# Kernel optimization log

Measured on AMD Instinct MI355X. Metric: run time of the kernel, lower is better.

## Reference

```python
import jax, jax.numpy as jnp
import numpy as np

N = 100000      # nodes
E = 1600000     # edges (avg degree 16)
IN, HID, OUT = 64, 64, 32
R = 8           # relations


def setup_inputs() -> dict:
    key = jax.random.key(0)
    ks = jax.random.split(key, 8)
    s = jnp.float32(0.05)  # weight init scale
    return {
        "feat": jax.random.normal(ks[0], (N, IN), dtype=jnp.float32),
        "src": jax.random.randint(ks[1], (E,), 0, N),
        "dst": jax.random.randint(ks[2], (E,), 0, N),
        "etypes": jax.random.randint(ks[3], (E,), 0, R),
        "W1": jax.random.normal(ks[4], (R, IN, HID), dtype=jnp.float32) * s,
        "Wself1": jax.random.normal(ks[5], (IN, HID), dtype=jnp.float32) * s,
        "b1": jnp.zeros((HID,), jnp.float32),
        "W2": jax.random.normal(ks[6], (R, HID, OUT), dtype=jnp.float32) * s,
        "Wself2": jax.random.normal(ks[7], (HID, OUT), dtype=jnp.float32) * s,
        "b2": jnp.zeros((OUT,), jnp.float32),
    }


def _rel_graph_conv(h, src, dst, etypes, W, Wself, b):
    """RelGraphConv with sum aggregation, self-loop and bias.

    h: [N, din], W: [R, din, dout], Wself: [din, dout], b: [dout].
    """
    n = h.shape[0]
    # Transform all nodes by all relation weights once: [R, N, dout].
    hW = jnp.einsum('nd,rdo->rno', h, W)
    # Per-edge message: relation-specific transform of the source node.
    msg = hW[etypes, src]                                    # [E, dout]
    # Scatter-add messages to destination nodes.
    agg = jax.ops.segment_sum(msg, dst, num_segments=n)      # [N, dout]
    return agg + h @ Wself + b


def reference(feat, src, dst, etypes, W1, Wself1, b1, W2, Wself2, b2):
    x = jax.nn.relu(_rel_graph_conv(feat, src, dst, etypes, W1, Wself1, b1))
    return _rel_graph_conv(x, src, dst, etypes, W2, Wself2, b2)
```

## Files before the change

kernel.cpp:

```cpp
#include <hip/hip_runtime.h>
#include <hip/hip_bf16.h>

typedef __attribute__((ext_vector_type(8))) short short8;
typedef __attribute__((ext_vector_type(4))) float f32x4;

__device__ __forceinline__ unsigned short f2bf(float v) {
    __hip_bfloat16 h = __float2bfloat16(v);
    return *reinterpret_cast<unsigned short*>(&h);
}
__device__ __forceinline__ float bf2f(unsigned short u) {
    union { unsigned int i; float f; } x;
    x.i = (unsigned int)u << 16;
    return x.f;
}

constexpr int MAXB = 2048;

template<int H>
__global__ __launch_bounds__(256) void transpose_w(
    const float* __restrict__ W, const float* __restrict__ Wself,
    unsigned short* __restrict__ Wt, int R)
{
    int i = blockIdx.x * 256 + threadIdx.x;
    int total = (R + 1) * H * 64;
    if (i >= total) return;
    int d = i & 63;
    int hh = i >> 6;
    int r = hh / H, h = hh % H;
    float v = (r < R) ? W[((size_t)r * 64 + d) * H + h]
                      : Wself[(size_t)d * H + h];
    Wt[i] = f2bf(v);
}

template<int H, int RT, bool ABF, bool SBF>
__global__ __launch_bounds__(512) void gemm_rel_mfma(
    const void* __restrict__ Av, const unsigned short* __restrict__ Wt,
    const float* __restrict__ bias,
    unsigned short* __restrict__ C, void* __restrict__ Cselfv,
    int N, int Rrt, int relu)
{
    constexpr int AS = 72;
    __shared__ unsigned short As[64 * AS];
    const int R = RT ? RT : Rrt;
    const int tid = threadIdx.x;
    const int n0 = blockIdx.x * 64;

    if constexpr (ABF) {
        const unsigned short* A = (const unsigned short*)Av;
        int n = tid >> 3, d8 = (tid & 7) * 8;
        int gn = n0 + n;
        short8 u = {};
        if (gn < N) u = *(const short8*)&A[(size_t)gn * 64 + d8];
        if (relu) {
            #pragma unroll
            for (int j = 0; j < 8; ++j) {
                unsigned short x = (unsigned short)u[j];
                u[j] = (short)((x & 0x8000) ? 0 : x);
            }
        }
        *(short8*)&As[n * AS + d8] = u;
    } else {
        const float* A = (const float*)Av;
        #pragma unroll
        for (int i = 0; i < 2; ++i) {
            int lin = tid + i * 512;
            int n = lin >> 4;
            int d4 = (lin & 15) * 4;
            int gn = n0 + n;
            float4 v = make_float4(0.f, 0.f, 0.f, 0.f);
            if (gn < N) v = *(const float4*)&A[(size_t)gn * 64 + d4];
            if (relu) {
                v.x = fmaxf(v.x, 0.f); v.y = fmaxf(v.y, 0.f);
                v.z = fmaxf(v.z, 0.f); v.w = fmaxf(v.w, 0.f);
            }
            ushort4 u;
            u.x = f2bf(v.x); u.y = f2bf(v.y); u.z = f2bf(v.z); u.w = f2bf(v.w);
            *(ushort4*)&As[n * AS + d4] = u;
        }
    }

    const int w = tid >> 6, lane = tid & 63;
    const int m = lane & 15, quad = lane >> 4;
    const int wt = w & 3;
    const int half = w >> 2;
    const int node = n0 + wt * 16 + m;

    __syncthreads();

    short8 afrag[2];
    afrag[0] = *(const short8*)&As[(wt * 16 + m) * AS + 0 * 32 + quad * 8];
    afrag[1] = *(const short8*)&As[(wt * 16 + m) * AS + 1 * 32 + quad * 8];

    constexpr int NT = H / 32;

    auto wptr = [&](int r, int nt, int kc) {
        int colbase = half * (H / 2) + nt * 16;
        return (const short8*)&Wt[((size_t)(r * H + colbase + m)) * 64 + kc * 32 + quad * 8];
    };

    short8 wf0[NT][2], wf1[NT][2];
    #pragma unroll
    for (int nt = 0; nt < NT; ++nt) { wf0[nt][0] = *wptr(0, nt, 0); wf0[nt][1] = *wptr(0, nt, 1); }
    #pragma unroll
    for (int nt = 0; nt < NT; ++nt) { wf1[nt][0] = *wptr(1, nt, 0); wf1[nt][1] = *wptr(1, nt, 1); }

    #pragma unroll
    for (int r = 0; r <= R; ++r) {
        short8 wn[NT][2];
        if (r + 2 <= R) {
            #pragma unroll
            for (int nt = 0; nt < NT; ++nt) {
                wn[nt][0] = *wptr(r + 2, nt, 0);
                wn[nt][1] = *wptr(r + 2, nt, 1);
            }
        }

        f32x4 acc[NT];
        #pragma unroll
        for (int nt = 0; nt < NT; ++nt) {
            acc[nt] = (f32x4){0.f, 0.f, 0.f, 0.f};
            acc[nt] = __builtin_amdgcn_mfma_f32_16x16x32_bf16(wf0[nt][0], afrag[0], acc[nt], 0, 0, 0);
            acc[nt] = __builtin_amdgcn_mfma_f32_16x16x32_bf16(wf0[nt][1], afrag[1], acc[nt], 0, 0, 0);
        }

        if (r < R) {
            #pragma unroll
            for (int nt = 0; nt < NT; ++nt) {
                int colbase = half * (H / 2) + nt * 16;
                if (node < N) {
                    ushort4 u;
                    u.x = f2bf(acc[nt][0]); u.y = f2bf(acc[nt][1]);
                    u.z = f2bf(acc[nt][2]); u.w = f2bf(acc[nt][3]);
                    *(ushort4*)&C[((size_t)r * N + node) * H + colbase + quad * 4] = u;
                }
            }
        } else {
            #pragma unroll
            for (int nt = 0; nt < NT; ++nt) {
                int colbase = half * (H / 2) + nt * 16;
                if (node < N) {
                    float4 bv = *(const float4*)&bias[colbase + quad * 4];
                    if constexpr (SBF) {
                        unsigned short* Cs = (unsigned short*)Cselfv;
                        ushort4 u;
                        u.x = f2bf(acc[nt][0] + bv.x); u.y = f2bf(acc[nt][1] + bv.y);
                        u.z = f2bf(acc[nt][2] + bv.z); u.w = f2bf(acc[nt][3] + bv.w);
                        *(ushort4*)&Cs[(size_t)node * H + colbase + quad * 4] = u;
                    } else {
                        float* Cs = (float*)Cselfv;
                        float4 o = make_float4(acc[nt][0] + bv.x, acc[nt][1] + bv.y,
                                               acc[nt][2] + bv.z, acc[nt][3] + bv.w);
                        *(float4*)&Cs[(size_t)node * H + colbase + quad * 4] = o;
                    }
                }
            }
        }

        #pragma unroll
        for (int nt = 0; nt < NT; ++nt) {
            wf0[nt][0] = wf1[nt][0]; wf0[nt][1] = wf1[nt][1];
            wf1[nt][0] = wn[nt][0];  wf1[nt][1] = wn[nt][1];
        }
    }
}

__global__ __launch_bounds__(256) void zero_int(int* __restrict__ p, int n) {
    int i = blockIdx.x * 256 + threadIdx.x;
    if (i < n) p[i] = 0;
}

__global__ __launch_bounds__(256) void fine_hist(
    const int* __restrict__ dst, int* __restrict__ ghist, int E, int B, int CH)
{
    __shared__ int hist[MAXB];
    const int t = threadIdx.x;
    const int e0 = blockIdx.x * CH, e1 = min(E, e0 + CH);
    for (int i = t; i < B; i += 256) hist[i] = 0;
    __syncthreads();
    for (int e = e0 + t; e < e1; e += 256) atomicAdd(&hist[dst[e] >> 6], 1);
    __syncthreads();
    for (int i = t; i < B; i += 256) {
        int h = hist[i];
        if (h) atomicAdd(&ghist[i], h);
    }
}

__global__ __launch_bounds__(256) void fine_scan(
    const int* __restrict__ ghist, int* __restrict__ bstart,
    int* __restrict__ cursor, int B, int E)
{
    __shared__ int ts[256];
    const int t = threadIdx.x;
    const int PER = (B + 255) / 256;
    int loc[8];
    int s = 0;
    for (int j = 0; j < PER; ++j) {
        int i = t * PER + j;
        loc[j] = (i < B) ? ghist[i] : 0;
        s += loc[j];
    }
    ts[t] = s;
    __syncthreads();
    for (int off = 1; off < 256; off <<= 1) {
        int x = (t >= off) ? ts[t - off] : 0;
        __syncthreads();
        ts[t] += x;
        __syncthreads();
    }
    int run = ts[t] - s;
    for (int j = 0; j < PER; ++j) {
        int i = t * PER + j;
        if (i < B) { bstart[i] = run; cursor[i] = run; }
        run += loc[j];
    }
    if (t == 255) bstart[B] = E;
}

__global__ __launch_bounds__(256) void partition_fine(
    const int* __restrict__ src, const int* __restrict__ dst,
    const int* __restrict__ et, int* __restrict__ cursor,
    int* __restrict__ rec, int E, int N, int B, int CH)
{
    __shared__ int hist[MAXB];
    __shared__ int base[MAXB];
    __shared__ int cnt[MAXB];
    const int t = threadIdx.x;
    const int e0 = blockIdx.x * CH, e1 = min(E, e0 + CH);

    for (int i = t; i < B; i += 256) hist[i] = 0;
    __syncthreads();
    for (int e = e0 + t; e < e1; e += 256) atomicAdd(&hist[dst[e] >> 6], 1);
    __syncthreads();
    for (int i = t; i < B; i += 256) {
        int h = hist[i];
        base[i] = h ? atomicAdd(&cursor[i], h) : 0;
        cnt[i] = 0;
    }
    __syncthreads();
    for (int e = e0 + t; e < e1; e += 256) {
        int d = dst[e];
        int b = d >> 6;
        int pos = base[b] + atomicAdd(&cnt[b], 1);
        rec[pos] = ((et[e] * N + src[e]) << 6) | (d & 63);
    }
}

__global__ __launch_bounds__(256) void bucket_sort(
    const int* __restrict__ bstart, const int* __restrict__ rec,
    int* __restrict__ eidx, int* __restrict__ row_ptr, int N, int E)
{
    __shared__ int hist[64];
    __shared__ int excl[64];
    __shared__ int cur[64];
    const int b = blockIdx.x;
    const int tid = threadIdx.x;
    const int p0 = bstart[b], p1 = bstart[b + 1];

    if (tid < 64) hist[tid] = 0;
    __syncthreads();
    for (int p = p0 + tid; p < p1; p += 256)
        atomicAdd(&hist[rec[p] & 63], 1);
    __syncthreads();
    if (tid == 0) {
        int run = 0;
        #pragma unroll
        for (int i = 0; i < 64; ++i) { excl[i] = run; run += hist[i]; }
    }
    __syncthreads();
    if (tid < 64) {
        cur[tid] = excl[tid];
        int n = b * 64 + tid;
        if (n < N) row_ptr[n] = p0 + excl[tid];
    }
    if (b == 0 && tid == 0) row_ptr[N] = E;
    __syncthreads();
    for (int p = p0 + tid; p < p1; p += 256) {
        int rv = rec[p];
        int pos = p0 + atomicAdd(&cur[rv & 63], 1);
        eidx[pos] = rv >> 6;
    }
}

__global__ __launch_bounds__(256) void agg_csr64(
    const unsigned int* __restrict__ hw32, const int* __restrict__ row_ptr,
    const int* __restrict__ eidx, unsigned int* __restrict__ out32, int N)
{
    const int d = blockIdx.x * 4 + (threadIdx.x >> 6);
    const int lane = threadIdx.x & 63;
    if (d >= N) return;
    const int he = lane >> 5;
    const int c = lane & 31;
    const int p0 = row_ptr[d], p1 = row_ptr[d + 1];
    float s0 = 0.f, s1 = 0.f, t0 = 0.f, t1 = 0.f;
    int p = p0 + he;
    for (; p + 6 < p1; p += 8) {
        unsigned int v0 = hw32[(size_t)eidx[p]     * 32 + c];
        unsigned int v1 = hw32[(size_t)eidx[p + 2] * 32 + c];
        unsigned int v2 = hw32[(size_t)eidx[p + 4] * 32 + c];
        unsigned int v3 = hw32[(size_t)eidx[p + 6] * 32 + c];
        s0 += bf2f((unsigned short)(v0 & 0xffff)); s1 += bf2f((unsigned short)(v0 >> 16));
        t0 += bf2f((unsigned short)(v1 & 0xffff)); t1 += bf2f((unsigned short)(v1 >> 16));
        s0 += bf2f((unsigned short)(v2 & 0xffff)); s1 += bf2f((unsigned short)(v2 >> 16));
        t0 += bf2f((unsigned short)(v3 & 0xffff)); t1 += bf2f((unsigned short)(v3 >> 16));
    }
    for (; p < p1; p += 2) {
        unsigned int v = hw32[(size_t)eidx[p] * 32 + c];
        s0 += bf2f((unsigned short)(v & 0xffff)); s1 += bf2f((unsigned short)(v >> 16));
    }
    s0 += t0; s1 += t1;
    float u0 = __shfl(s0, c + 32, 64);
    float u1 = __shfl(s1, c + 32, 64);
    if (he == 0) {
        unsigned int cur = out32[(size_t)d * 32 + c];
        float o0 = s0 + u0 + bf2f((unsigned short)(cur & 0xffff));
        float o1 = s1 + u1 + bf2f((unsigned short)(cur >> 16));
        out32[(size_t)d * 32 + c] = (unsigned int)f2bf(o0) | ((unsigned int)f2bf(o1) << 16);
    }
}

__global__ __launch_bounds__(256) void agg_csr32(
    const unsigned int* __restrict__ hw32, const int* __restrict__ row_ptr,
    const int* __restrict__ eidx, float* __restrict__ out, int N)
{
    const int d = blockIdx.x * 8 + (threadIdx.x >> 5);
    const int l = threadIdx.x & 31;
    if (d >= N) return;
    const int he = l >> 4;
    const int c = l & 15;
    const int p0 = row_ptr[d], p1 = row_ptr[d + 1];
    float s0 = 0.f, s1 = 0.f, t0 = 0.f, t1 = 0.f;
    int p = p0 + he;
    for (; p + 6 < p1; p += 8) {
        unsigned int v0 = hw32[(size_t)eidx[p]     * 16 + c];
        unsigned int v1 = hw32[(size_t)eidx[p + 2] * 16 + c];
        unsigned int v2 = hw32[(size_t)eidx[p + 4] * 16 + c];
        unsigned int v3 = hw32[(size_t)eidx[p + 6] * 16 + c];
        s0 += bf2f((unsigned short)(v0 & 0xffff)); s1 += bf2f((unsigned short)(v0 >> 16));
        t0 += bf2f((unsigned short)(v1 & 0xffff)); t1 += bf2f((unsigned short)(v1 >> 16));
        s0 += bf2f((unsigned short)(v2 & 0xffff)); s1 += bf2f((unsigned short)(v2 >> 16));
        t0 += bf2f((unsigned short)(v3 & 0xffff)); t1 += bf2f((unsigned short)(v3 >> 16));
    }
    for (; p < p1; p += 2) {
        unsigned int v = hw32[(size_t)eidx[p] * 16 + c];
        s0 += bf2f((unsigned short)(v & 0xffff)); s1 += bf2f((unsigned short)(v >> 16));
    }
    s0 += t0; s1 += t1;
    float u0 = __shfl(s0, (threadIdx.x & 63) ^ 16, 64);
    float u1 = __shfl(s1, (threadIdx.x & 63) ^ 16, 64);
    if (he == 0) {
        float2 cur = *(const float2*)&out[(size_t)d * 32 + c * 2];
        float2 o = make_float2(cur.x + s0 + u0, cur.y + s1 + u1);
        *(float2*)&out[(size_t)d * 32 + c * 2] = o;
    }
}

extern "C" void kernel_launch(void* const* d_in, const int* in_sizes, int n_in,
                              void* d_out, int out_size, void* d_ws, size_t ws_size,
                              hipStream_t stream)
{
    const float* feat = (const float*)d_in[0];
    const int*   src  = (const int*)d_in[1];
    const int*   dst  = (const int*)d_in[2];
    const int*   et   = (const int*)d_in[3];
    const float* W1   = (const float*)d_in[4];
    const float* Ws1  = (const float*)d_in[5];
    const float* b1   = (const float*)d_in[6];
    const float* W2   = (const float*)d_in[7];
    const float* Ws2  = (const float*)d_in[8];
    const float* b2   = (const float*)d_in[9];
    float* out = (float*)d_out;

    const int N = in_sizes[0] / 64;
    const int E = in_sizes[1];
    const int R = in_sizes[4] / (64 * 64);
    const int B = (N + 63) / 64;

    unsigned short* hW  = (unsigned short*)d_ws;
    unsigned short* h1  = hW + (size_t)R * N * 64;
    unsigned short* Wt1 = h1 + (size_t)N * 64;
    unsigned short* Wt2 = Wt1 + (size_t)(R + 1) * 64 * 64;
    int*   ghist   = (int*)(Wt2 + (size_t)(R + 1) * 32 * 64);
    int*   bstart  = ghist + B;
    int*   cursor  = bstart + (B + 1);
    int*   row_ptr = cursor + B;
    int*   rec     = row_ptr + (N + 1);
    int*   eidx    = rec + E;

    const dim3 blk(256);
    const int nblk64 = (N + 63) / 64;
    const int P  = 128;
    const int CH = (E + P - 1) / P;

    transpose_w<64><<<((R + 1) * 64 * 64 + 255) / 256, blk, 0, stream>>>(W1, Ws1, Wt1, R);
    transpose_w<32><<<((R + 1) * 32 * 64 + 255) / 256, blk, 0, stream>>>(W2, Ws2, Wt2, R);

    zero_int<<<(B + 255) / 256, blk, 0, stream>>>(ghist, B);
    fine_hist<<<P, blk, 0, stream>>>(dst, ghist, E, B, CH);
    fine_scan<<<1, blk, 0, stream>>>(ghist, bstart, cursor, B, E);
    partition_fine<<<P, blk, 0, stream>>>(src, dst, et, cursor, rec, E, N, B, CH);
    bucket_sort<<<B, blk, 0, stream>>>(bstart, rec, eidx, row_ptr, N, E);

    if (R == 8)
        gemm_rel_mfma<64, 8, false, true><<<nblk64, 512, 0, stream>>>(feat, Wt1, b1, hW, h1, N, R, 0);
    else
        gemm_rel_mfma<64, 0, false, true><<<nblk64, 512, 0, stream>>>(feat, Wt1, b1, hW, h1, N, R, 0);
    agg_csr64<<<dim3((N + 3) / 4), blk, 0, stream>>>((const unsigned int*)hW, row_ptr, eidx,
                                                     (unsigned int*)h1, N);

    if (R == 8)
        gemm_rel_mfma<32, 8, true, false><<<nblk64, 512, 0, stream>>>(h1, Wt2, b2, hW, out, N, R, 1);
    else
        gemm_rel_mfma<32, 0, true, false><<<nblk64, 512, 0, stream>>>(h1, Wt2, b2, hW, out, N, R, 1);
    agg_csr32<<<dim3((N + 7) / 8), blk, 0, stream>>>((const unsigned int*)hW, row_ptr, eidx, out, N);
}
```

Before: 396.3 us.

## Aggregate source features per relation before transform, fusing gather and GEMM

Reorders the RGCN layer to aggregate raw bf16 source features per (destination tile, relation) into shared memory with LDS atomics, then multiply by each relation weight with MFMA. This drops materialising the R×N×H transformed-feature tensor and its separate gather pass. Edges are bucketed by destination tile and then by relation, and the packed record now stores etype in high bits. The cost is shared-memory atomics, many block syncs per relation, and bf16 rounding of the partial sums before the MFMA.

```diff
diff --git a/kernel.cpp b/kernel.cpp
--- a/kernel.cpp
+++ b/kernel.cpp
@@ -15,6 +15,7 @@
 }
 
 constexpr int MAXB = 2048;
+constexpr int SP   = 66;
 
 template<int H>
 __global__ __launch_bounds__(256) void transpose_w(
@@ -32,136 +33,19 @@
     Wt[i] = f2bf(v);
 }
 
-template<int H, int RT, bool ABF, bool SBF>
-__global__ __launch_bounds__(512) void gemm_rel_mfma(
-    const void* __restrict__ Av, const unsigned short* __restrict__ Wt,
-    const float* __restrict__ bias,
-    unsigned short* __restrict__ C, void* __restrict__ Cselfv,
-    int N, int Rrt, int relu)
-{
-    constexpr int AS = 72;
-    __shared__ unsigned short As[64 * AS];
-    const int R = RT ? RT : Rrt;
-    const int tid = threadIdx.x;
-    const int n0 = blockIdx.x * 64;
-
-    if constexpr (ABF) {
-        const unsigned short* A = (const unsigned short*)Av;
-        int n = tid >> 3, d8 = (tid & 7) * 8;
-        int gn = n0 + n;
-        short8 u = {};
-        if (gn < N) u = *(const short8*)&A[(size_t)gn * 64 + d8];
-        if (relu) {
-            #pragma unroll
-            for (int j = 0; j < 8; ++j) {
-                unsigned short x = (unsigned short)u[j];
-                u[j] = (short)((x & 0x8000) ? 0 : x);
-            }
-        }
-        *(short8*)&As[n * AS + d8] = u;
-    } else {
-        const float* A = (const float*)Av;
-        #pragma unroll
-        for (int i = 0; i < 2; ++i) {
-            int lin = tid + i * 512;
-            int n = lin >> 4;
-            int d4 = (lin & 15) * 4;
-            int gn = n0 + n;
-            float4 v = make_float4(0.f, 0.f, 0.f, 0.f);
-            if (gn < N) v = *(const float4*)&A[(size_t)gn * 64 + d4];
-            if (relu) {
-                v.x = fmaxf(v.x, 0.f); v.y = fmaxf(v.y, 0.f);
-                v.z = fmaxf(v.z, 0.f); v.w = fmaxf(v.w, 0.f);
-            }
-            ushort4 u;
-            u.x = f2bf(v.x); u.y = f2bf(v.y); u.z = f2bf(v.z); u.w = f2bf(v.w);
-            *(ushort4*)&As[n * AS + d4] = u;
-        }
-    }
-
-    const int w = tid >> 6, lane = tid & 63;
-    const int m = lane & 15, quad = lane >> 4;
-    const int wt = w & 3;
-    const int half = w >> 2;
-    const int node = n0 + wt * 16 + m;
-
-    __syncthreads();
-
-    short8 afrag[2];
-    afrag[0] = *(const short8*)&As[(wt * 16 + m) * AS + 0 * 32 + quad * 8];
-    afrag[1] = *(const short8*)&As[(wt * 16 + m) * AS + 1 * 32 + quad * 8];
-
-    constexpr int NT = H / 32;
-
-    auto wptr = [&](int r, int nt, int kc) {
-        int colbase = half * (H / 2) + nt * 16;
-        return (const short8*)&Wt[((size_t)(r * H + colbase + m)) * 64 + kc * 32 + quad * 8];
-    };
-
-    short8 wf0[NT][2], wf1[NT][2];
-    #pragma unroll
-    for (int nt = 0; nt < NT; ++nt) { wf0[nt][0] = *wptr(0, nt, 0); wf0[nt][1] = *wptr(0, nt, 1); }
-    #pragma unroll
-    for (int nt = 0; nt < NT; ++nt) { wf1[nt][0] = *wptr(1, nt, 0); wf1[nt][1] = *wptr(1, nt, 1); }
-
-    #pragma unroll
-    for (int r = 0; r <= R; ++r) {
-        short8 wn[NT][2];
-        if (r + 2 <= R) {
-            #pragma unroll
-            for (int nt = 0; nt < NT; ++nt) {
-                wn[nt][0] = *wptr(r + 2, nt, 0);
-                wn[nt][1] = *wptr(r + 2, nt, 1);
-            }
-        }
-
-        f32x4 acc[NT];
-        #pragma unroll
-        for (int nt = 0; nt < NT; ++nt) {
-            acc[nt] = (f32x4){0.f, 0.f, 0.f, 0.f};
-            acc[nt] = __builtin_amdgcn_mfma_f32_16x16x32_bf16(wf0[nt][0], afrag[0], acc[nt], 0, 0, 0);
-            acc[nt] = __builtin_amdgcn_mfma_f32_16x16x32_bf16(wf0[nt][1], afrag[1], acc[nt], 0, 0, 0);
-        }
-
-        if (r < R) {
-            #pragma unroll
-            for (int nt = 0; nt < NT; ++nt) {
-                int colbase = half * (H / 2) + nt * 16;
-                if (node < N) {
-                    ushort4 u;
-                    u.x = f2bf(acc[nt][0]); u.y = f2bf(acc[nt][1]);
-                    u.z = f2bf(acc[nt][2]); u.w = f2bf(acc[nt][3]);
-                    *(ushort4*)&C[((size_t)r * N + node) * H + colbase + quad * 4] = u;
-                }
-            }
-        } else {
-            #pragma unroll
-            for (int nt = 0; nt < NT; ++nt) {
-                int colbase = half * (H / 2) + nt * 16;
-                if (node < N) {
-                    float4 bv = *(const float4*)&bias[colbase + quad * 4];
-                    if constexpr (SBF) {
-                        unsigned short* Cs = (unsigned short*)Cselfv;
-                        ushort4 u;
-                        u.x = f2bf(acc[nt][0] + bv.x); u.y = f2bf(acc[nt][1] + bv.y);
-                        u.z = f2bf(acc[nt][2] + bv.z); u.w = f2bf(acc[nt][3] + bv.w);
-                        *(ushort4*)&Cs[(size_t)node * H + colbase + quad * 4] = u;
-                    } else {
-                        float* Cs = (float*)Cselfv;
-                        float4 o = make_float4(acc[nt][0] + bv.x, acc[nt][1] + bv.y,
-                                               acc[nt][2] + bv.z, acc[nt][3] + bv.w);
-                        *(float4*)&Cs[(size_t)node * H + colbase + quad * 4] = o;
-                    }
-                }
-            }
-        }
-
-        #pragma unroll
-        for (int nt = 0; nt < NT; ++nt) {
-            wf0[nt][0] = wf1[nt][0]; wf0[nt][1] = wf1[nt][1];
-            wf1[nt][0] = wn[nt][0];  wf1[nt][1] = wn[nt][1];
-        }
-    }
+__global__ __launch_bounds__(256) void cast_bf16x8(
+    const float* __restrict__ in, unsigned short* __restrict__ outp, int n8)
+{
+    int i = blockIdx.x * 256 + threadIdx.x;
+    if (i >= n8) return;
+    const float4 a = ((const float4*)in)[(size_t)i * 2];
+    const float4 b = ((const float4*)in)[(size_t)i * 2 + 1];
+    short8 u;
+    u[0] = (short)f2bf(a.x); u[1] = (short)f2bf(a.y);
+    u[2] = (short)f2bf(a.z); u[3] = (short)f2bf(a.w);
+    u[4] = (short)f2bf(b.x); u[5] = (short)f2bf(b.y);
+    u[6] = (short)f2bf(b.z); u[7] = (short)f2bf(b.w);
+    *(short8*)&outp[(size_t)i * 8] = u;
 }
 
 __global__ __launch_bounds__(256) void zero_int(int* __restrict__ p, int n) {
@@ -241,116 +125,205 @@
         int d = dst[e];
         int b = d >> 6;
         int pos = base[b] + atomicAdd(&cnt[b], 1);
-        rec[pos] = ((et[e] * N + src[e]) << 6) | (d & 63);
-    }
-}
-
-__global__ __launch_bounds__(256) void bucket_sort(
+        rec[pos] = (et[e] << 23) | (src[e] << 6) | (d & 63);
+    }
+}
+
+__global__ __launch_bounds__(256) void bucket_sort_rel(
     const int* __restrict__ bstart, const int* __restrict__ rec,
-    int* __restrict__ eidx, int* __restrict__ row_ptr, int N, int E)
-{
-    __shared__ int hist[64];
-    __shared__ int excl[64];
-    __shared__ int cur[64];
+    int* __restrict__ eidx, int* __restrict__ brp, int R)
+{
+    __shared__ int hist[16];
+    __shared__ int excl[17];
+    __shared__ int cur[16];
     const int b = blockIdx.x;
     const int tid = threadIdx.x;
     const int p0 = bstart[b], p1 = bstart[b + 1];
 
-    if (tid < 64) hist[tid] = 0;
+    if (tid < 16) hist[tid] = 0;
     __syncthreads();
     for (int p = p0 + tid; p < p1; p += 256)
-        atomicAdd(&hist[rec[p] & 63], 1);
+        atomicAdd(&hist[rec[p] >> 23], 1);
     __syncthreads();
     if (tid == 0) {
         int run = 0;
-        #pragma unroll
-        for (int i = 0; i < 64; ++i) { excl[i] = run; run += hist[i]; }
-    }
-    __syncthreads();
-    if (tid < 64) {
-        cur[tid] = excl[tid];
-        int n = b * 64 + tid;
-        if (n < N) row_ptr[n] = p0 + excl[tid];
-    }
-    if (b == 0 && tid == 0) row_ptr[N] = E;
+        for (int i = 0; i < R; ++i) { excl[i] = run; run += hist[i]; }
+        excl[R] = run;
+    }
+    __syncthreads();
+    if (tid <= R) {
+        brp[b * (R + 1) + tid] = p0 + excl[tid];
+        if (tid < R) cur[tid] = excl[tid];
+    }
     __syncthreads();
     for (int p = p0 + tid; p < p1; p += 256) {
         int rv = rec[p];
-        int pos = p0 + atomicAdd(&cur[rv & 63], 1);
-        eidx[pos] = rv >> 6;
-    }
-}
-
-__global__ __launch_bounds__(256) void agg_csr64(
-    const unsigned int* __restrict__ hw32, const int* __restrict__ row_ptr,
-    const int* __restrict__ eidx, unsigned int* __restrict__ out32, int N)
-{
-    const int d = blockIdx.x * 4 + (threadIdx.x >> 6);
-    const int lane = threadIdx.x & 63;
-    if (d >= N) return;
-    const int he = lane >> 5;
-    const int c = lane & 31;
-    const int p0 = row_ptr[d], p1 = row_ptr[d + 1];
-    float s0 = 0.f, s1 = 0.f, t0 = 0.f, t1 = 0.f;
-    int p = p0 + he;
-    for (; p + 6 < p1; p += 8) {
-        unsigned int v0 = hw32[(size_t)eidx[p]     * 32 + c];
-        unsigned int v1 = hw32[(size_t)eidx[p + 2] * 32 + c];
-        unsigned int v2 = hw32[(size_t)eidx[p + 4] * 32 + c];
-        unsigned int v3 = hw32[(size_t)eidx[p + 6] * 32 + c];
-        s0 += bf2f((unsigned short)(v0 & 0xffff)); s1 += bf2f((unsigned short)(v0 >> 16));
-        t0 += bf2f((unsigned short)(v1 & 0xffff)); t1 += bf2f((unsigned short)(v1 >> 16));
-        s0 += bf2f((unsigned short)(v2 & 0xffff)); s1 += bf2f((unsigned short)(v2 >> 16));
-        t0 += bf2f((unsigned short)(v3 & 0xffff)); t1 += bf2f((unsigned short)(v3 >> 16));
-    }
-    for (; p < p1; p += 2) {
-        unsigned int v = hw32[(size_t)eidx[p] * 32 + c];
-        s0 += bf2f((unsigned short)(v & 0xffff)); s1 += bf2f((unsigned short)(v >> 16));
-    }
-    s0 += t0; s1 += t1;
-    float u0 = __shfl(s0, c + 32, 64);
-    float u1 = __shfl(s1, c + 32, 64);
-    if (he == 0) {
-        unsigned int cur = out32[(size_t)d * 32 + c];
-        float o0 = s0 + u0 + bf2f((unsigned short)(cur & 0xffff));
-        float o1 = s1 + u1 + bf2f((unsigned short)(cur >> 16));
-        out32[(size_t)d * 32 + c] = (unsigned int)f2bf(o0) | ((unsigned int)f2bf(o1) << 16);
-    }
-}
-
-__global__ __launch_bounds__(256) void agg_csr32(
-    const unsigned int* __restrict__ hw32, const int* __restrict__ row_ptr,
-    const int* __restrict__ eidx, float* __restrict__ out, int N)
-{
-    const int d = blockIdx.x * 8 + (threadIdx.x >> 5);
-    const int l = threadIdx.x & 31;
-    if (d >= N) return;
-    const int he = l >> 4;
-    const int c = l & 15;
-    const int p0 = row_ptr[d], p1 = row_ptr[d + 1];
-    float s0 = 0.f, s1 = 0.f, t0 = 0.f, t1 = 0.f;
-    int p = p0 + he;
-    for (; p + 6 < p1; p += 8) {
-        unsigned int v0 = hw32[(size_t)eidx[p]     * 16 + c];
-        unsigned int v1 = hw32[(size_t)eidx[p + 2] * 16 + c];
-        unsigned int v2 = hw32[(size_t)eidx[p + 4] * 16 + c];
-        unsigned int v3 = hw32[(size_t)eidx[p + 6] * 16 + c];
-        s0 += bf2f((unsigned short)(v0 & 0xffff)); s1 += bf2f((unsigned short)(v0 >> 16));
-        t0 += bf2f((unsigned short)(v1 & 0xffff)); t1 += bf2f((unsigned short)(v1 >> 16));
-        s0 += bf2f((unsigned short)(v2 & 0xffff)); s1 += bf2f((unsigned short)(v2 >> 16));
-        t0 += bf2f((unsigned short)(v3 & 0xffff)); t1 += bf2f((unsigned short)(v3 >> 16));
-    }
-    for (; p < p1; p += 2) {
-        unsigned int v = hw32[(size_t)eidx[p] * 16 + c];
-        s0 += bf2f((unsigned short)(v & 0xffff)); s1 += bf2f((unsigned short)(v >> 16));
-    }
-    s0 += t0; s1 += t1;
-    float u0 = __shfl(s0, (threadIdx.x & 63) ^ 16, 64);
-    float u1 = __shfl(s1, (threadIdx.x & 63) ^ 16, 64);
-    if (he == 0) {
-        float2 cur = *(const float2*)&out[(size_t)d * 32 + c * 2];
-        float2 o = make_float2(cur.x + s0 + u0, cur.y + s1 + u1);
-        *(float2*)&out[(size_t)d * 32 + c * 2] = o;
+        int pos = p0 + atomicAdd(&cur[rv >> 23], 1);
+        eidx[pos] = rv & 0x7FFFFF;
+    }
+}
+
+__device__ __forceinline__ void agg_range(
+    const unsigned int* __restrict__ in32, const int* __restrict__ eidx,
+    float* __restrict__ S, int q0, int q1, int hwv, int c)
+{
+    int p = q0 + hwv;
+    for (; p + 24 < q1; p += 32) {
+        int r0 = eidx[p], r1 = eidx[p + 8], r2 = eidx[p + 16], r3 = eidx[p + 24];
+        unsigned int v0 = in32[(size_t)(r0 >> 6) * 32 + c];
+        unsigned int v1 = in32[(size_t)(r1 >> 6) * 32 + c];
+        unsigned int v2 = in32[(size_t)(r2 >> 6) * 32 + c];
+        unsigned int v3 = in32[(size_t)(r3 >> 6) * 32 + c];
+        int b0 = (r0 & 63) * SP + 2 * c;
+        int b1 = (r1 & 63) * SP + 2 * c;
+        int b2 = (r2 & 63) * SP + 2 * c;
+        int b3 = (r3 & 63) * SP + 2 * c;
+        atomicAdd(&S[b0],     bf2f((unsigned short)(v0 & 0xffff)));
+        atomicAdd(&S[b0 + 1], bf2f((unsigned short)(v0 >> 16)));
+        atomicAdd(&S[b1],     bf2f((unsigned short)(v1 & 0xffff)));
+        atomicAdd(&S[b1 + 1], bf2f((unsigned short)(v1 >> 16)));
+        atomicAdd(&S[b2],     bf2f((unsigned short)(v2 & 0xffff)));
+        atomicAdd(&S[b2 + 1], bf2f((unsigned short)(v2 >> 16)));
+        atomicAdd(&S[b3],     bf2f((unsigned short)(v3 & 0xffff)));
+        atomicAdd(&S[b3 + 1], bf2f((unsigned short)(v3 >> 16)));
+    }
+    for (; p < q1; p += 8) {
+        int r0 = eidx[p];
+        unsigned int v0 = in32[(size_t)(r0 >> 6) * 32 + c];
+        int b0 = (r0 & 63) * SP + 2 * c;
+        atomicAdd(&S[b0],     bf2f((unsigned short)(v0 & 0xffff)));
+        atomicAdd(&S[b0 + 1], bf2f((unsigned short)(v0 >> 16)));
+    }
+}
+
+template<int HOUT, bool BF16OUT>
+__global__ __launch_bounds__(256) void fused_layer(
+    const unsigned short* __restrict__ inb,
+    const unsigned short* __restrict__ Wt,
+    const float* __restrict__ bias,
+    const int* __restrict__ brp,
+    const int* __restrict__ eidx,
+    void* __restrict__ outp,
+    int N, int R)
+{
+    alignas(16) __shared__ float S[64 * SP];
+    __shared__ int qs[17];
+
+    const unsigned int* in32 = (const unsigned int*)inb;
+    const int b = blockIdx.x;
+    const int tid = threadIdx.x;
+    const int n0 = b * 64;
+    const int w = tid >> 6, lane = tid & 63;
+    const int m = lane & 15, quad = lane >> 4;
+    const int hwv = tid >> 5, c = tid & 31;
+
+    if (tid <= R) qs[tid] = brp[b * (R + 1) + tid];
+    {
+        f32x4 z = {0.f, 0.f, 0.f, 0.f};
+        for (int i = tid; i < 64 * SP / 4; i += 256) ((f32x4*)S)[i] = z;
+    }
+    __syncthreads();
+
+    agg_range(in32, eidx, S, qs[0], qs[1], hwv, c);
+    __syncthreads();
+
+    constexpr int NT = HOUT / 16;
+    f32x4 acc[NT];
+    #pragma unroll
+    for (int nt = 0; nt < NT; ++nt) acc[nt] = (f32x4){0.f, 0.f, 0.f, 0.f};
+
+    auto wptr = [&](int r, int nt, int kc) {
+        return (const short8*)&Wt[((size_t)(r * HOUT + nt * 16 + m)) * 64 + kc * 32 + quad * 8];
+    };
+
+    for (int r = 0; r < R; ++r) {
+        short8 sf0, sf1;
+        const float* Srow = &S[(w * 16 + m) * SP + quad * 8];
+        #pragma unroll
+        for (int j = 0; j < 8; ++j) sf0[j] = (short)f2bf(Srow[j]);
+        #pragma unroll
+        for (int j = 0; j < 8; ++j) sf1[j] = (short)f2bf(Srow[32 + j]);
+
+        #pragma unroll
+        for (int nt = 0; nt < NT; ++nt) {
+            short8 wa = *wptr(r, nt, 0);
+            short8 wb = *wptr(r, nt, 1);
+            acc[nt] = __builtin_amdgcn_mfma_f32_16x16x32_bf16(wa, sf0, acc[nt], 0, 0, 0);
+            acc[nt] = __builtin_amdgcn_mfma_f32_16x16x32_bf16(wb, sf1, acc[nt], 0, 0, 0);
+        }
+
+        __syncthreads();
+        if (r + 1 < R) {
+            f32x4 z = {0.f, 0.f, 0.f, 0.f};
+            for (int i = tid; i < 64 * SP / 4; i += 256) ((f32x4*)S)[i] = z;
+            __syncthreads();
+            agg_range(in32, eidx, S, qs[r + 1], qs[r + 2], hwv, c);
+            __syncthreads();
+        }
+    }
+
+    const int node = n0 + w * 16 + m;
+    short8 se0 = {}, se1 = {};
+    if (node < N) {
+        se0 = *(const short8*)&inb[(size_t)node * 64 + quad * 8];
+        se1 = *(const short8*)&inb[(size_t)node * 64 + 32 + quad * 8];
+    }
+    #pragma unroll
+    for (int nt = 0; nt < NT; ++nt) {
+        short8 wa = *wptr(R, nt, 0);
+        short8 wb = *wptr(R, nt, 1);
+        acc[nt] = __builtin_amdgcn_mfma_f32_16x16x32_bf16(wa, se0, acc[nt], 0, 0, 0);
+        acc[nt] = __builtin_amdgcn_mfma_f32_16x16x32_bf16(wb, se1, acc[nt], 0, 0, 0);
+    }
+
+    if constexpr (BF16OUT) {
+        unsigned int* Su = (unsigned int*)S;
+        const int row = w * 16 + m;
+        #pragma unroll
+        for (int nt = 0; nt < NT; ++nt) {
+            const float4 bv = *(const float4*)&bias[nt * 16 + quad * 4];
+            float o0 = fmaxf(acc[nt][0] + bv.x, 0.f);
+            float o1 = fmaxf(acc[nt][1] + bv.y, 0.f);
+            float o2 = fmaxf(acc[nt][2] + bv.z, 0.f);
+            float o3 = fmaxf(acc[nt][3] + bv.w, 0.f);
+            int colu = (nt * 16 + quad * 4) >> 1;
+            Su[row * 36 + colu]     = (unsigned int)f2bf(o0) | ((unsigned int)f2bf(o1) << 16);
+            Su[row * 36 + colu + 1] = (unsigned int)f2bf(o2) | ((unsigned int)f2bf(o3) << 16);
+        }
+        __syncthreads();
+        unsigned int* outu = (unsigned int*)outp;
+        #pragma unroll
+        for (int it = 0; it < 2; ++it) {
+            int i = tid + it * 256;
+            int rw = i >> 3, ch = i & 7;
+            int gn = n0 + rw;
+            if (gn < N) {
+                uint4 v = *(const uint4*)&Su[rw * 36 + ch * 4];
+                *(uint4*)&outu[(size_t)gn * 32 + ch * 4] = v;
+            }
+        }
+    } else {
+        float* Sf = S;
+        const int row = w * 16 + m;
+        #pragma unroll
+        for (int nt = 0; nt < NT; ++nt) {
+            const float4 bv = *(const float4*)&bias[nt * 16 + quad * 4];
+            float4 o = make_float4(acc[nt][0] + bv.x, acc[nt][1] + bv.y,
+                                   acc[nt][2] + bv.z, acc[nt][3] + bv.w);
+            *(float4*)&Sf[row * 36 + nt * 16 + quad * 4] = o;
+        }
+        __syncthreads();
+        float* outf = (float*)outp;
+        #pragma unroll
+        for (int it = 0; it < 2; ++it) {
+            int i = tid + it * 256;
+            int rw = i >> 3, ch = i & 7;
+            int gn = n0 + rw;
+            if (gn < N) {
+                float4 v = *(const float4*)&Sf[rw * 36 + ch * 4];
+                *(float4*)&outf[(size_t)gn * 32 + ch * 4] = v;
+            }
+        }
     }
 }
 
@@ -375,41 +348,33 @@
     const int R = in_sizes[4] / (64 * 64);
     const int B = (N + 63) / 64;
 
-    unsigned short* hW  = (unsigned short*)d_ws;
-    unsigned short* h1  = hW + (size_t)R * N * 64;
-    unsigned short* Wt1 = h1 + (size_t)N * 64;
-    unsigned short* Wt2 = Wt1 + (size_t)(R + 1) * 64 * 64;
-    int*   ghist   = (int*)(Wt2 + (size_t)(R + 1) * 32 * 64);
-    int*   bstart  = ghist + B;
-    int*   cursor  = bstart + (B + 1);
-    int*   row_ptr = cursor + B;
-    int*   rec     = row_ptr + (N + 1);
-    int*   eidx    = rec + E;
+    unsigned short* fstage = (unsigned short*)d_ws;
+    unsigned short* h1     = fstage + (size_t)N * 64;
+    unsigned short* Wt1    = h1 + (size_t)N * 64;
+    unsigned short* Wt2    = Wt1 + (size_t)(R + 1) * 64 * 64;
+    int* ghist   = (int*)(Wt2 + (size_t)(R + 1) * 32 * 64);
+    int* bstart  = ghist + B;
+    int* cursor  = bstart + (B + 1);
+    int* brp     = cursor + B;
+    int* rec     = brp + (size_t)B * (R + 1);
+    int* eidx    = rec + E;
 
     const dim3 blk(256);
-    const int nblk64 = (N + 63) / 64;
     const int P  = 128;
     const int CH = (E + P - 1) / P;
+    const int n8 = N * 64 / 8;
 
     transpose_w<64><<<((R + 1) * 64 * 64 + 255) / 256, blk, 0, stream>>>(W1, Ws1, Wt1, R);
     transpose_w<32><<<((R + 1) * 32 * 64 + 255) / 256, blk, 0, stream>>>(W2, Ws2, Wt2, R);
+    cast_bf16x8<<<(n8 + 255) / 256, blk, 0, stream>>>(feat, fstage, n8);
 
     zero_int<<<(B + 255) / 256, blk, 0, stream>>>(ghist, B);
     fine_hist<<<P, blk, 0, stream>>>(dst, ghist, E, B, CH);
     fine_scan<<<1, blk, 0, stream>>>(ghist, bstart, cursor, B, E);
     partition_fine<<<P, blk, 0, stream>>>(src, dst, et, cursor, rec, E, N, B, CH);
-    bucket_sort<<<B, blk, 0, stream>>>(bstart, rec, eidx, row_ptr, N, E);
-
-    if (R == 8)
-        gemm_rel_mfma<64, 8, false, true><<<nblk64, 512, 0, stream>>>(feat, Wt1, b1, hW, h1, N, R, 0);
-    else
-        gemm_rel_mfma<64, 0, false, true><<<nblk64, 512, 0, stream>>>(feat, Wt1, b1, hW, h1, N, R, 0);
-    agg_csr64<<<dim3((N + 3) / 4), blk, 0, stream>>>((const unsigned int*)hW, row_ptr, eidx,
-                                                     (unsigned int*)h1, N);
-
-    if (R == 8)
-        gemm_rel_mfma<32, 8, true, false><<<nblk64, 512, 0, stream>>>(h1, Wt2, b2, hW, out, N, R, 1);
-    else
-        gemm_rel_mfma<32, 0, true, false><<<nblk64, 512, 0, stream>>>(h1, Wt2, b2, hW, out, N, R, 1);
-    agg_csr32<<<dim3((N + 7) / 8), blk, 0, stream>>>((const unsigned int*)hW, row_ptr, eidx, out, N);
-}
+    bucket_sort_rel<<<B, blk, 0, stream>>>(bstart, rec, eidx, brp, R);
+
+    fused_layer<64, true><<<B, blk, 0, stream>>>(fstage, Wt1, b1, brp, eidx, h1, N, R);
+
+    fused_layer<32, false><<<B, blk, 0, stream>>>(h1, Wt2, b2, brp, eidx, out, N, R);
+}
```

After: 1.414 ms. +256.9%, slower.
